# Optimization experiments

Hardware: AMD Instinct MI355X
Metric: run time of the kernel (lower is better)

Reference implementation:

```python
import jax, jax.numpy as jnp
import numpy as np

D_MODEL = 1024
N_HEADS = 16
HEAD_DIM = D_MODEL // N_HEADS


def setup_inputs() -> dict:
    key = jax.random.key(0)
    ks = jax.random.split(key, 6)
    B, S = 2, 2048
    scale = 1.0 / np.sqrt(D_MODEL)
    x = jax.random.normal(ks[0], (B, S, D_MODEL), dtype=jnp.float32)
    Wq = jax.random.normal(ks[1], (D_MODEL, D_MODEL), dtype=jnp.float32) * scale
    Wk = jax.random.normal(ks[2], (D_MODEL, D_MODEL), dtype=jnp.float32) * scale
    Wv = jax.random.normal(ks[3], (D_MODEL, D_MODEL), dtype=jnp.float32) * scale
    Wo = jax.random.normal(ks[4], (D_MODEL, D_MODEL), dtype=jnp.float32) * scale
    bo = jax.random.normal(ks[5], (D_MODEL,), dtype=jnp.float32) * 0.02
    return {"x": x, "Wq": Wq, "Wk": Wk, "Wv": Wv, "Wo": Wo, "bo": bo}


def reference(x, Wq, Wk, Wv, Wo, bo):
    B, S, _ = x.shape
    H, hd = N_HEADS, HEAD_DIM
    # qkv projections (no bias, qkv_bias=False)
    q = (x @ Wq).reshape(B, S, H, hd).transpose(0, 2, 1, 3)  # [B,H,S,hd]
    k = (x @ Wk).reshape(B, S, H, hd).transpose(0, 2, 1, 3)
    v = (x @ Wv).reshape(B, S, H, hd).transpose(0, 2, 1, 3)
    scores = jnp.einsum('bhqd,bhkd->bhqk', q, k)  # [B,H,S,S]
    causal = jnp.tril(jnp.ones((S, S), dtype=bool))  # True = keep
    scores = jnp.where(causal, scores, -jnp.inf)
    weights = jax.nn.softmax(scores / np.sqrt(hd), axis=-1)
    # dropout p=0.0 -> identity
    ctx = jnp.einsum('bhqk,bhkd->bhqd', weights, v)  # [B,H,S,hd]
    ctx = ctx.transpose(0, 2, 1, 3).reshape(B, S, H * hd)
    return ctx @ Wo + bo
```

## Files before the change

### kernel.cpp

```cpp
#include <hip/hip_runtime.h>
#include <hip/hip_bf16.h>
#include <stdint.h>

#define SEQ    2048
#define BATCH  2
#define DMODEL 1024
#define NHEADS 16
#define HDIM   64
#define MROWS  (BATCH*SEQ)

typedef __attribute__((ext_vector_type(8))) short bf16x8;
typedef __attribute__((ext_vector_type(4))) short bf16x4;
typedef __attribute__((ext_vector_type(4))) float f32x4;

__device__ inline void global_to_lds16(const void* g, void* l) {
  __builtin_amdgcn_global_load_lds(
      (const __attribute__((address_space(1))) uint32_t*)g,
      (__attribute__((address_space(3))) uint32_t*)l, 16, 0, 0);
}

__device__ inline unsigned short f2bf_bits(float f) {
  __hip_bfloat16 h = __float2bfloat16(f);
  return *(unsigned short*)&h;
}

__global__ void prep_kernel(const float* __restrict__ x, __hip_bfloat16* __restrict__ xb,
                            const float* __restrict__ Wq, const float* __restrict__ Wk,
                            const float* __restrict__ Wv, const float* __restrict__ Wo,
                            __hip_bfloat16* __restrict__ Wqkv_t, __hip_bfloat16* __restrict__ Wo_t) {
  __shared__ float tile[32][33];
  if (blockIdx.x < 4096) {
    int i = (blockIdx.x * 256 + threadIdx.x) * 4;
    float4 v = *(const float4*)(x + i);
    ushort4 o;
    o.x = f2bf_bits(v.x); o.y = f2bf_bits(v.y);
    o.z = f2bf_bits(v.z); o.w = f2bf_bits(v.w);
    *(ushort4*)(xb + i) = o;
    return;
  }
  int idx = blockIdx.x - 4096;
  int z = idx >> 10;
  int rem = idx & 1023;
  const float* W = (z == 0) ? Wq : (z == 1) ? Wk : (z == 2) ? Wv : Wo;
  __hip_bfloat16* dst = (z < 3) ? (Wqkv_t + (size_t)z * 1024 * 1024) : Wo_t;
  int k0 = (rem & 31) * 32, n0 = (rem >> 5) * 32;
  int tx = threadIdx.x & 31, ty = threadIdx.x >> 5;
#pragma unroll
  for (int r = 0; r < 4; r++)
    tile[ty + r * 8][tx] = W[(size_t)(k0 + ty + r * 8) * 1024 + n0 + tx];
  __syncthreads();
#pragma unroll
  for (int r = 0; r < 4; r++)
    dst[(size_t)(n0 + ty + r * 8) * 1024 + k0 + tx] = __float2bfloat16(tile[tx][ty + r * 8]);
}

template <int TN, bool OUT_BF16, int MINW, bool FUSE_VT>
__global__ __launch_bounds__(256, MINW)
void gemm_kernel(const __hip_bfloat16* __restrict__ A, const __hip_bfloat16* __restrict__ Bt,
                 void* __restrict__ C, const float* __restrict__ bias, int ldc,
                 __hip_bfloat16* __restrict__ Vt) {
  __shared__ __hip_bfloat16 Asl[128 * 64];
  __shared__ __hip_bfloat16 Bsl[TN * 64];

  const int t = threadIdx.x;
  const int lane = t & 63;
  const int w = t >> 6;
  constexpr int MI = (TN == 128) ? 4 : 2;
  const int wrow = (TN == 128) ? (w >> 1) * 64 : w * 32;
  const int wcol = (TN == 128) ? (w & 1) * 64 : 0;
  const int m0 = blockIdx.y * 128;
  const int n0 = blockIdx.x * TN;

  f32x4 acc[MI][4];
#pragma unroll
  for (int i = 0; i < MI; i++)
#pragma unroll
    for (int j = 0; j < 4; j++) acc[i][j] = (f32x4){0.f, 0.f, 0.f, 0.f};

  const int srow = lane >> 3;
  const int sjc = (lane & 7) ^ srow;
  const int fm = lane & 15;
  const int g4 = lane >> 4;

  for (int k0 = 0; k0 < 1024; k0 += 64) {
#pragma unroll
    for (int i = 0; i < 4; i++) {
      int seg = i * 4 + w;
      int r = seg * 8 + srow;
      global_to_lds16(A + (size_t)(m0 + r) * 1024 + k0 + sjc * 8,
                      (void*)(Asl + seg * 512 + lane * 8));
    }
#pragma unroll
    for (int i = 0; i < TN / 32; i++) {
      int seg = i * 4 + w;
      int r = seg * 8 + srow;
      global_to_lds16(Bt + (size_t)(n0 + r) * 1024 + k0 + sjc * 8,
                      (void*)(Bsl + seg * 512 + lane * 8));
    }
    __syncthreads();
#pragma unroll
    for (int kb = 0; kb < 2; kb++) {
      bf16x8 af[MI], bfr[4];
#pragma unroll
      for (int mi = 0; mi < MI; mi++) {
        int row = wrow + mi * 16 + fm;
        af[mi] = *(const bf16x8*)(Asl + row * 64 + (((kb * 4 + g4) ^ (row & 7)) << 3));
      }
#pragma unroll
      for (int ni = 0; ni < 4; ni++) {
        int row = wcol + ni * 16 + fm;
        bfr[ni] = *(const bf16x8*)(Bsl + row * 64 + (((kb * 4 + g4) ^ (row & 7)) << 3));
      }
#pragma unroll
      for (int mi = 0; mi < MI; mi++)
#pragma unroll
        for (int ni = 0; ni < 4; ni++)
          acc[mi][ni] = __builtin_amdgcn_mfma_f32_16x16x32_bf16(af[mi], bfr[ni], acc[mi][ni], 0, 0, 0);
    }
    __syncthreads();
  }

  const bool vt_block = FUSE_VT && (n0 >= 2048);
#pragma unroll
  for (int mi = 0; mi < MI; mi++) {
    int mb = m0 + wrow + mi * 16 + g4 * 4;
#pragma unroll
    for (int ni = 0; ni < 4; ni++) {
      int n = n0 + wcol + ni * 16 + fm;
      if (vt_block) {
        int nv = n - 2048;
        int bhh = (mb >> 11) * 16 + (nv >> 6);
        int d = nv & 63;
        int s = mb & 2047;
        unsigned short u[4];
#pragma unroll
        for (int r = 0; r < 4; r++) u[r] = f2bf_bits(acc[mi][ni][r]);
        *(ushort4*)(Vt + ((size_t)bhh * 64 + d) * 2048 + s) = *(const ushort4*)u;
      } else {
        float bv = OUT_BF16 ? 0.f : bias[n];
#pragma unroll
        for (int r = 0; r < 4; r++) {
          if (OUT_BF16)
            ((__hip_bfloat16*)C)[(size_t)(mb + r) * ldc + n] = __float2bfloat16(acc[mi][ni][r]);
          else
            ((float*)C)[(size_t)(mb + r) * ldc + n] = acc[mi][ni][r] + bv;
        }
      }
    }
  }
}

__global__ __launch_bounds__(256, 3)
void attn_kernel(const __hip_bfloat16* __restrict__ QKV,
                 const __hip_bfloat16* __restrict__ Vt,
                 __hip_bfloat16* __restrict__ ctx) {
  __shared__ __hip_bfloat16 Klds[2][64 * 64];
  __shared__ __hip_bfloat16 Vlds[2][64 * 64];

  const int t = threadIdx.x;
  const int lane = t & 63;
  const int w = t >> 6;
  const int L = blockIdx.x;
  const int bh = (L & 7) + 8 * ((L >> 3) & 3);
  const int qt = 31 - (L >> 5);
  const int b = bh >> 4, h = bh & 15;
  const int fm = lane & 15;
  const int g4 = lane >> 4;
  const int fk = g4 * 8;
  const size_t rowb = (size_t)b * SEQ;
  const float c = 0.18033688011112042f;

  const int krr = lane >> 3;
  const int kjc = (lane & 7) ^ krr;

  bf16x8 qf[2];
  {
    const __hip_bfloat16* qp = QKV + (rowb + qt * 64 + w * 16 + fm) * 3072 + h * 64 + fk;
    bf16x8 r0 = *(const bf16x8*)qp;
    bf16x8 r1 = *(const bf16x8*)(qp + 32);
#pragma unroll
    for (int i = 0; i < 8; i++) {
      float f0 = __uint_as_float(((unsigned)(unsigned short)r0[i]) << 16) * c;
      float f1 = __uint_as_float(((unsigned)(unsigned short)r1[i]) << 16) * c;
      r0[i] = (short)f2bf_bits(f0);
      r1[i] = (short)f2bf_bits(f1);
    }
    qf[0] = r0; qf[1] = r1;
  }

  bf16x4 ones4;
#pragma unroll
  for (int i = 0; i < 4; i++) ones4[i] = (short)0x3F80;

  f32x4 acc[4];
  f32x4 lacc = (f32x4){0.f, 0.f, 0.f, 0.f};
#pragma unroll
  for (int d = 0; d < 4; d++) acc[d] = (f32x4){0.f, 0.f, 0.f, 0.f};

  auto stage = [&](int kts, int bufi) {
    const int kt0 = kts * 64;
#pragma unroll
    for (int i = 0; i < 2; i++) {
      int seg = w + i * 4;
      int r = seg * 8 + krr;
      global_to_lds16(QKV + (rowb + kt0 + r) * 3072 + 1024 + h * 64 + kjc * 8,
                      (void*)(&Klds[bufi][0] + seg * 512 + lane * 8));
      global_to_lds16(Vt + ((size_t)bh * 64 + r) * 2048 + kt0 + kjc * 8,
                      (void*)(&Vlds[bufi][0] + seg * 512 + lane * 8));
    }
  };

  stage(0, 0);
  for (int kts = 0; kts <= qt; ++kts) {
    __syncthreads();
    if (kts < qt) stage(kts + 1, (kts + 1) & 1);
    const __hip_bfloat16* Kb = &Klds[kts & 1][0];
    const __hip_bfloat16* Vb = &Vlds[kts & 1][0];

    f32x4 st[4];
#pragma unroll
    for (int ns = 0; ns < 4; ns++) st[ns] = (f32x4){0.f, 0.f, 0.f, 0.f};
#pragma unroll
    for (int kk = 0; kk < 2; kk++) {
#pragma unroll
      for (int ns = 0; ns < 4; ns++) {
        bf16x8 kf = *(const bf16x8*)(Kb + (ns * 16 + fm) * 64 + (((kk * 4 + g4) ^ (fm & 7)) << 3));
        st[ns] = __builtin_amdgcn_mfma_f32_16x16x32_bf16(kf, qf[kk], st[ns], 0, 0, 0);
      }
    }

    bf16x4 vf[4][4];
#pragma unroll
    for (int dd = 0; dd < 4; dd++)
#pragma unroll
      for (int ns = 0; ns < 4; ns++)
        vf[dd][ns] = *(const bf16x4*)(Vb + (dd * 16 + fm) * 64 +
                                      (((2 * ns + (g4 >> 1)) ^ (fm & 7)) << 3) + (g4 & 1) * 4);

    const bool diag = (kts == qt);
#pragma unroll
    for (int ns = 0; ns < 4; ns++) {
      float e[4];
#pragma unroll
      for (int r = 0; r < 4; r++) {
        float p = __builtin_amdgcn_exp2f(st[ns][r]);
        if (diag) {
          int ktl = ns * 16 + g4 * 4 + r;
          p = (ktl > w * 16 + fm) ? 0.f : p;
        }
        e[r] = p;
      }
      unsigned lo = __builtin_amdgcn_perm(__builtin_bit_cast(unsigned, e[1]),
                                          __builtin_bit_cast(unsigned, e[0]), 0x07060302u);
      unsigned hi = __builtin_amdgcn_perm(__builtin_bit_cast(unsigned, e[3]),
                                          __builtin_bit_cast(unsigned, e[2]), 0x07060302u);
      uint2 pp; pp.x = lo; pp.y = hi;
      bf16x4 pf = __builtin_bit_cast(bf16x4, pp);
      lacc = __builtin_amdgcn_mfma_f32_16x16x16bf16_1k(pf, ones4, lacc, 0, 0, 0);
#pragma unroll
      for (int dd = 0; dd < 4; dd++)
        acc[dd] = __builtin_amdgcn_mfma_f32_16x16x16bf16_1k(pf, vf[dd][ns], acc[dd], 0, 0, 0);
    }
  }

  float rl[4];
#pragma unroll
  for (int r = 0; r < 4; r++) rl[r] = __builtin_amdgcn_rcpf(lacc[r]);
#pragma unroll
  for (int dd = 0; dd < 4; dd++)
#pragma unroll
    for (int r = 0; r < 4; r++) {
      int q = qt * 64 + w * 16 + g4 * 4 + r;
      ctx[(rowb + q) * 1024 + h * 64 + dd * 16 + fm] =
          __float2bfloat16(acc[dd][r] * rl[r]);
    }
}

extern "C" void kernel_launch(void* const* d_in, const int* in_sizes, int n_in,
                              void* d_out, int out_size, void* d_ws, size_t ws_size,
                              hipStream_t stream) {
  const float* x  = (const float*)d_in[0];
  const float* Wq = (const float*)d_in[1];
  const float* Wk = (const float*)d_in[2];
  const float* Wv = (const float*)d_in[3];
  const float* Wo = (const float*)d_in[4];
  const float* bo = (const float*)d_in[5];
  float* out = (float*)d_out;

  char* ws = (char*)d_ws;
  __hip_bfloat16* xb     = (__hip_bfloat16*)(ws);
  __hip_bfloat16* Wqkv_t = (__hip_bfloat16*)(ws + (8ull  << 20));
  __hip_bfloat16* Wo_t   = (__hip_bfloat16*)(ws + (14ull << 20));
  __hip_bfloat16* QKV    = (__hip_bfloat16*)(ws + (16ull << 20));
  __hip_bfloat16* ctxb   = (__hip_bfloat16*)(ws + (40ull << 20));
  __hip_bfloat16* Vt     = (__hip_bfloat16*)(ws + (48ull << 20));

  prep_kernel<<<dim3(8192), dim3(256), 0, stream>>>(x, xb, Wq, Wk, Wv, Wo, Wqkv_t, Wo_t);
  gemm_kernel<128, true, 3, true><<<dim3(24, 32), dim3(256), 0, stream>>>(
      xb, Wqkv_t, (void*)QKV, nullptr, 3072, Vt);
  attn_kernel<<<dim3(1024), dim3(256), 0, stream>>>(QKV, Vt, ctxb);
  gemm_kernel<64, false, 2, false><<<dim3(16, 32), dim3(256), 0, stream>>>(
      ctxb, Wo_t, (void*)out, bo, 1024, nullptr);
}
```

Before: 169.0 us.

## Use 128-query tiles with 8 waves per attention block sharing K/V staging

The attention kernel now processes 128 query rows per block with 512 threads (8 waves), halving the grid and letting each staged 64-row K/V tile be reused by twice as many waves. Staging is done with one load per thread, and waves whose causal range ends earlier skip compute on later tiles while still joining the barriers. This cuts global K/V traffic per query, but the lower half of waves idle on the final tile. Fewer, larger blocks also change the occupancy and load-balance tradeoff.

```diff
diff --git a/kernel.cpp b/kernel.cpp
--- a/kernel.cpp
+++ b/kernel.cpp
@@ -150,7 +150,7 @@
   }
 }
 
-__global__ __launch_bounds__(256, 3)
+__global__ __launch_bounds__(512, 4)
 void attn_kernel(const __hip_bfloat16* __restrict__ QKV,
                  const __hip_bfloat16* __restrict__ Vt,
                  __hip_bfloat16* __restrict__ ctx) {
@@ -162,7 +162,7 @@
   const int w = t >> 6;
   const int L = blockIdx.x;
   const int bh = (L & 7) + 8 * ((L >> 3) & 3);
-  const int qt = 31 - (L >> 5);
+  const int qt = 15 - (L >> 5);
   const int b = bh >> 4, h = bh & 15;
   const int fm = lane & 15;
   const int g4 = lane >> 4;
@@ -170,12 +170,16 @@
   const size_t rowb = (size_t)b * SEQ;
   const float c = 0.18033688011112042f;
 
-  const int krr = lane >> 3;
-  const int kjc = (lane & 7) ^ krr;
+  const int sr = t >> 3;
+  const int sjc = (t & 7) ^ (sr & 7);
+
+  const int qlo = qt * 128 + w * 16;
+  const int mtile = (qlo + 15) >> 6;
+  const int mbase = (w & 3) * 16;
 
   bf16x8 qf[2];
   {
-    const __hip_bfloat16* qp = QKV + (rowb + qt * 64 + w * 16 + fm) * 3072 + h * 64 + fk;
+    const __hip_bfloat16* qp = QKV + (rowb + qlo + fm) * 3072 + h * 64 + fk;
     bf16x8 r0 = *(const bf16x8*)qp;
     bf16x8 r1 = *(const bf16x8*)(qp + 32);
 #pragma unroll
@@ -199,21 +203,18 @@
 
   auto stage = [&](int kts, int bufi) {
     const int kt0 = kts * 64;
-#pragma unroll
-    for (int i = 0; i < 2; i++) {
-      int seg = w + i * 4;
-      int r = seg * 8 + krr;
-      global_to_lds16(QKV + (rowb + kt0 + r) * 3072 + 1024 + h * 64 + kjc * 8,
-                      (void*)(&Klds[bufi][0] + seg * 512 + lane * 8));
-      global_to_lds16(Vt + ((size_t)bh * 64 + r) * 2048 + kt0 + kjc * 8,
-                      (void*)(&Vlds[bufi][0] + seg * 512 + lane * 8));
-    }
+    global_to_lds16(QKV + (rowb + kt0 + sr) * 3072 + 1024 + h * 64 + sjc * 8,
+                    (void*)(&Klds[bufi][0] + t * 8));
+    global_to_lds16(Vt + ((size_t)bh * 64 + sr) * 2048 + kt0 + sjc * 8,
+                    (void*)(&Vlds[bufi][0] + t * 8));
   };
 
+  const int lastt = 2 * qt + 1;
   stage(0, 0);
-  for (int kts = 0; kts <= qt; ++kts) {
+  for (int kts = 0; kts <= lastt; ++kts) {
     __syncthreads();
-    if (kts < qt) stage(kts + 1, (kts + 1) & 1);
+    if (kts < lastt) stage(kts + 1, (kts + 1) & 1);
+    if (kts > mtile) continue;
     const __hip_bfloat16* Kb = &Klds[kts & 1][0];
     const __hip_bfloat16* Vb = &Vlds[kts & 1][0];
 
@@ -237,7 +238,7 @@
         vf[dd][ns] = *(const bf16x4*)(Vb + (dd * 16 + fm) * 64 +
                                       (((2 * ns + (g4 >> 1)) ^ (fm & 7)) << 3) + (g4 & 1) * 4);
 
-    const bool diag = (kts == qt);
+    const bool diag = (kts == mtile);
 #pragma unroll
     for (int ns = 0; ns < 4; ns++) {
       float e[4];
@@ -246,7 +247,7 @@
         float p = __builtin_amdgcn_exp2f(st[ns][r]);
         if (diag) {
           int ktl = ns * 16 + g4 * 4 + r;
-          p = (ktl > w * 16 + fm) ? 0.f : p;
+          p = (ktl > mbase + fm) ? 0.f : p;
         }
         e[r] = p;
       }
@@ -270,7 +271,7 @@
   for (int dd = 0; dd < 4; dd++)
 #pragma unroll
     for (int r = 0; r < 4; r++) {
-      int q = qt * 64 + w * 16 + g4 * 4 + r;
+      int q = qlo + g4 * 4 + r;
       ctx[(rowb + q) * 1024 + h * 64 + dd * 16 + fm] =
           __float2bfloat16(acc[dd][r] * rl[r]);
     }
@@ -298,7 +299,7 @@
   prep_kernel<<<dim3(8192), dim3(256), 0, stream>>>(x, xb, Wq, Wk, Wv, Wo, Wqkv_t, Wo_t);
   gemm_kernel<128, true, 3, true><<<dim3(24, 32), dim3(256), 0, stream>>>(
       xb, Wqkv_t, (void*)QKV, nullptr, 3072, Vt);
-  attn_kernel<<<dim3(1024), dim3(256), 0, stream>>>(QKV, Vt, ctxb);
+  attn_kernel<<<dim3(512), dim3(512), 0, stream>>>(QKV, Vt, ctxb);
   gemm_kernel<64, false, 2, false><<<dim3(16, 32), dim3(256), 0, stream>>>(
       ctxb, Wo_t, (void*)out, bo, 1024, nullptr);
 }
```

Measured after the change: 173.9 us. +2.9%, slower.
